# Kernel optimization log

Hardware: AMD Instinct MI355X
Metric: run time of the kernel (lower is better)

The kernel has to match this reference:

```python
import jax, jax.numpy as jnp
import numpy as np

D_MODEL = 1024
D_FF = 4096
LN_EPS = 1e-5


def setup_inputs() -> dict:
    key = jax.random.key(0)
    k_x, k_w1, k_w2 = jax.random.split(key, 3)
    x = jax.random.normal(k_x, (4, 2048, D_MODEL), dtype=jnp.float32)
    # LayerNorm affine params (torch defaults: weight=1, bias=0)
    ln_w = jnp.ones((D_MODEL,), dtype=jnp.float32)
    ln_b = jnp.zeros((D_MODEL,), dtype=jnp.float32)
    # Linear layers, torch default init: U(-1/sqrt(fan_in), 1/sqrt(fan_in))
    lim1 = 1.0 / np.sqrt(D_MODEL)
    w1 = jax.random.uniform(k_w1, (D_MODEL, D_FF), minval=-lim1, maxval=lim1, dtype=jnp.float32)
    b1 = jnp.zeros((D_FF,), dtype=jnp.float32)
    lim2 = 1.0 / np.sqrt(D_FF)
    w2 = jax.random.uniform(k_w2, (D_FF, D_MODEL), minval=-lim2, maxval=lim2, dtype=jnp.float32)
    b2 = jnp.zeros((D_MODEL,), dtype=jnp.float32)
    return {"x": x, "ln_w": ln_w, "ln_b": ln_b, "w1": w1, "b1": b1, "w2": w2, "b2": b2}


def reference(x, ln_w, ln_b, w1, b1, w2, b2):
    # LayerNorm over last dim
    mu = jnp.mean(x, axis=-1, keepdims=True)
    var = jnp.mean(jnp.square(x - mu), axis=-1, keepdims=True)
    h = (x - mu) * jax.lax.rsqrt(var + LN_EPS) * ln_w + ln_b
    # Linear -> ReLU -> Linear
    h = jnp.maximum(jnp.einsum('bsd,df->bsf', h, w1) + b1, 0.0)
    return jnp.einsum('bsf,fd->bsd', h, w2) + b2
```

## Files before the change

### kernel.cpp

```cpp
#include <hip/hip_runtime.h>
#include <stdint.h>

#define D_MODEL 1024
#define D_FF    4096
#define NROWS   8192

typedef __attribute__((ext_vector_type(4))) float f32x4;
typedef __attribute__((ext_vector_type(8))) short short8;

__device__ __forceinline__ unsigned short f2bf(float f) {
  unsigned u = __float_as_uint(f);
  u += 0x7fffu + ((u >> 16) & 1u);
  return (unsigned short)(u >> 16);
}

__global__ __launch_bounds__(256) void ln_bf16_kernel(
    const float* __restrict__ x, const float* __restrict__ lnw,
    const float* __restrict__ lnb, unsigned short* __restrict__ y) {
  const int row = blockIdx.x;
  const int t = threadIdx.x;
  const int w = t >> 6, l = t & 63;
  const float4* xr = (const float4*)(x + (size_t)row * D_MODEL);
  float4 v = xr[t];
  float s  = v.x + v.y + v.z + v.w;
  float s2 = v.x * v.x + v.y * v.y + v.z * v.z + v.w * v.w;
#pragma unroll
  for (int o = 32; o >= 1; o >>= 1) {
    s  += __shfl_xor(s, o);
    s2 += __shfl_xor(s2, o);
  }
  __shared__ float red[8];
  if (l == 0) { red[w] = s; red[4 + w] = s2; }
  __syncthreads();
  s  = red[0] + red[1] + red[2] + red[3];
  s2 = red[4] + red[5] + red[6] + red[7];
  const float mu  = s * (1.0f / D_MODEL);
  const float var = s2 * (1.0f / D_MODEL) - mu * mu;
  const float rs  = rsqrtf(var + 1e-5f);
  float4 wv = ((const float4*)lnw)[t];
  float4 bv = ((const float4*)lnb)[t];
  ushort4 o4;
  o4.x = f2bf((v.x - mu) * rs * wv.x + bv.x);
  o4.y = f2bf((v.y - mu) * rs * wv.y + bv.y);
  o4.z = f2bf((v.z - mu) * rs * wv.z + bv.z);
  o4.w = f2bf((v.w - mu) * rs * wv.w + bv.w);
  *(ushort4*)(y + (size_t)row * D_MODEL + t * 4) = o4;
}

__global__ __launch_bounds__(256) void transpose_f32_bf16(
    const float* __restrict__ src, unsigned short* __restrict__ dst,
    int R, int C) {
  __shared__ float tile[32][33];
  const int tx = threadIdx.x;
  const int ty = threadIdx.y;
  const int r0 = blockIdx.y * 32, c0 = blockIdx.x * 32;
#pragma unroll
  for (int i = 0; i < 32; i += 8)
    tile[ty + i][tx] = src[(size_t)(r0 + ty + i) * C + (c0 + tx)];
  __syncthreads();
#pragma unroll
  for (int i = 0; i < 32; i += 8)
    dst[(size_t)(c0 + ty + i) * R + (r0 + tx)] = f2bf(tile[tx][ty + i]);
}

template <int RELU, int BF16OUT>
__global__ __launch_bounds__(256, 3) void gemm_bt(
    const unsigned short* __restrict__ A, const unsigned short* __restrict__ Bt,
    const float* __restrict__ bias, unsigned short* __restrict__ Cb,
    float* __restrict__ Cf, int M, int N, int K) {
  constexpr int BM = 128, BN = 128, BK = 64;
  __shared__ short lA[BM * BK];
  __shared__ short lB[BN * BK];
  const int t = threadIdx.x;
  const int w = t >> 6, l = t & 63;
  const int bm0 = blockIdx.y * BM, bn0 = blockIdx.x * BN;
  const int wm = (w >> 1) * 64, wn = (w & 1) * 64;

  f32x4 acc[4][4];
  const f32x4 zero = {0.f, 0.f, 0.f, 0.f};
#pragma unroll
  for (int i = 0; i < 4; ++i)
#pragma unroll
    for (int j = 0; j < 4; ++j) acc[i][j] = zero;

  const int nkt = K / BK;
  for (int kt = 0; kt < nkt; ++kt) {
    const int k0 = kt * BK;
#pragma unroll
    for (int p = 0; p < 4; ++p) {
      const int eb = (((p * 4 + w) * 64) + l) * 8;
      const int r = eb >> 6, c = eb & 63;
      __builtin_amdgcn_global_load_lds(
          (const __attribute__((address_space(1))) void*)(A + (size_t)(bm0 + r) * K + (k0 + c)),
          (__attribute__((address_space(3))) void*)(&lA[eb]), 16, 0, 0);
      __builtin_amdgcn_global_load_lds(
          (const __attribute__((address_space(1))) void*)(Bt + (size_t)(bn0 + r) * K + (k0 + c)),
          (__attribute__((address_space(3))) void*)(&lB[eb]), 16, 0, 0);
    }
    __syncthreads();

    const short8* pA = (const short8*)lA;
    const short8* pB = (const short8*)lB;
#pragma unroll
    for (int kb = 0; kb < 2; ++kb) {
      short8 af[4], bfr[4];
      const int kc = kb * 4 + (l >> 4);
#pragma unroll
      for (int f = 0; f < 4; ++f) {
        af[f]  = pA[(wm + f * 16 + (l & 15)) * 8 + kc];
        bfr[f] = pB[(wn + f * 16 + (l & 15)) * 8 + kc];
      }
#pragma unroll
      for (int fm = 0; fm < 4; ++fm)
#pragma unroll
        for (int fn = 0; fn < 4; ++fn)
          acc[fm][fn] = __builtin_amdgcn_mfma_f32_16x16x32_bf16(
              af[fm], bfr[fn], acc[fm][fn], 0, 0, 0);
    }
    __syncthreads();
  }

#pragma unroll
  for (int fn = 0; fn < 4; ++fn) {
    const int n = bn0 + wn + fn * 16 + (l & 15);
    const float bv = bias[n];
#pragma unroll
    for (int fm = 0; fm < 4; ++fm) {
      const int mbase = bm0 + wm + fm * 16 + ((l >> 4) * 4);
#pragma unroll
      for (int j = 0; j < 4; ++j) {
        float v = acc[fm][fn][j] + bv;
        if (RELU) v = v > 0.f ? v : 0.f;
        if (BF16OUT) Cb[(size_t)(mbase + j) * N + n] = f2bf(v);
        else         Cf[(size_t)(mbase + j) * N + n] = v;
      }
    }
  }
}

extern "C" void kernel_launch(void* const* d_in, const int* in_sizes, int n_in,
                              void* d_out, int out_size, void* d_ws, size_t ws_size,
                              hipStream_t stream) {
  const float* x   = (const float*)d_in[0];
  const float* lnw = (const float*)d_in[1];
  const float* lnb = (const float*)d_in[2];
  const float* w1  = (const float*)d_in[3];
  const float* b1  = (const float*)d_in[4];
  const float* w2  = (const float*)d_in[5];
  const float* b2  = (const float*)d_in[6];
  float* out = (float*)d_out;

  char* ws = (char*)d_ws;
  unsigned short* x_ln = (unsigned short*)(ws);
  unsigned short* w1t  = (unsigned short*)(ws + (16u << 20));
  unsigned short* w2t  = (unsigned short*)(ws + (24u << 20));
  unsigned short* h    = (unsigned short*)(ws + (32u << 20));

  ln_bf16_kernel<<<NROWS, 256, 0, stream>>>(x, lnw, lnb, x_ln);
  transpose_f32_bf16<<<dim3(D_FF / 32, D_MODEL / 32), dim3(32, 8), 0, stream>>>(
      w1, w1t, D_MODEL, D_FF);
  transpose_f32_bf16<<<dim3(D_MODEL / 32, D_FF / 32), dim3(32, 8), 0, stream>>>(
      w2, w2t, D_FF, D_MODEL);
  gemm_bt<1, 1><<<dim3(D_FF / 128, NROWS / 128), 256, 0, stream>>>(
      x_ln, w1t, b1, h, nullptr, NROWS, D_FF, D_MODEL);
  gemm_bt<0, 0><<<dim3(D_MODEL / 128, NROWS / 128), 256, 0, stream>>>(
      h, w2t, b2, nullptr, out, NROWS, D_MODEL, D_FF);
}
```

Before: 284.8 us.

## Double-buffer LDS in second GEMM and remap workgroups across XCDs

Adds a PREFETCH template option that double-buffers the A/B LDS tiles, so the next K-tile's global_load_lds is issued before the current tile's MFMAs run, with one barrier per iteration. It is enabled only for the second GEMM (K=4096), and that variant's occupancy hint drops from 3 to 2 blocks because it needs twice the LDS. Both GEMMs also get a workgroup-ID remap that gives each group of 8 consecutive hardware IDs (interleaved across XCDs) a contiguous tile range, for better L2 locality. Risks are lower occupancy and a waitcnt that may stall on the just-issued prefetch before the MFMAs drain.

```diff
diff --git a/kernel.cpp b/kernel.cpp
--- a/kernel.cpp
+++ b/kernel.cpp
@@ -63,17 +63,25 @@
     dst[(size_t)(c0 + ty + i) * R + (r0 + tx)] = f2bf(tile[tx][ty + i]);
 }
 
-template <int RELU, int BF16OUT>
-__global__ __launch_bounds__(256, 3) void gemm_bt(
+template <int RELU, int BF16OUT, int PREFETCH>
+__global__ __launch_bounds__(256, PREFETCH ? 2 : 3) void gemm_bt(
     const unsigned short* __restrict__ A, const unsigned short* __restrict__ Bt,
     const float* __restrict__ bias, unsigned short* __restrict__ Cb,
     float* __restrict__ Cf, int M, int N, int K) {
   constexpr int BM = 128, BN = 128, BK = 64;
-  __shared__ short lA[BM * BK];
-  __shared__ short lB[BN * BK];
+  constexpr int NBUF = PREFETCH ? 2 : 1;
+  __shared__ short lA[NBUF * BM * BK];
+  __shared__ short lB[NBUF * BN * BK];
   const int t = threadIdx.x;
   const int w = t >> 6, l = t & 63;
-  const int bm0 = blockIdx.y * BM, bn0 = blockIdx.x * BN;
+
+  const int gx = gridDim.x;
+  const int nwg = gx * gridDim.y;
+  int id = blockIdx.y * gx + blockIdx.x;
+  id = (id & 7) * (nwg >> 3) + (id >> 3);
+  const int bn0 = (id % gx) * BN;
+  const int bm0 = (id / gx) * BM;
+
   const int wm = (w >> 1) * 64, wn = (w & 1) * 64;
 
   f32x4 acc[4][4];
@@ -83,24 +91,25 @@
 #pragma unroll
     for (int j = 0; j < 4; ++j) acc[i][j] = zero;
 
-  const int nkt = K / BK;
-  for (int kt = 0; kt < nkt; ++kt) {
+  auto stage = [&](int buf, int kt) {
     const int k0 = kt * BK;
+    const int bo = buf * BM * BK;
 #pragma unroll
     for (int p = 0; p < 4; ++p) {
       const int eb = (((p * 4 + w) * 64) + l) * 8;
       const int r = eb >> 6, c = eb & 63;
       __builtin_amdgcn_global_load_lds(
           (const __attribute__((address_space(1))) void*)(A + (size_t)(bm0 + r) * K + (k0 + c)),
-          (__attribute__((address_space(3))) void*)(&lA[eb]), 16, 0, 0);
+          (__attribute__((address_space(3))) void*)(&lA[bo + eb]), 16, 0, 0);
       __builtin_amdgcn_global_load_lds(
           (const __attribute__((address_space(1))) void*)(Bt + (size_t)(bn0 + r) * K + (k0 + c)),
-          (__attribute__((address_space(3))) void*)(&lB[eb]), 16, 0, 0);
+          (__attribute__((address_space(3))) void*)(&lB[bo + eb]), 16, 0, 0);
     }
-    __syncthreads();
+  };
 
-    const short8* pA = (const short8*)lA;
-    const short8* pB = (const short8*)lB;
+  auto compute = [&](int buf) {
+    const short8* pA = (const short8*)&lA[buf * BM * BK];
+    const short8* pB = (const short8*)&lB[buf * BN * BK];
 #pragma unroll
     for (int kb = 0; kb < 2; ++kb) {
       short8 af[4], bfr[4];
@@ -117,7 +126,29 @@
           acc[fm][fn] = __builtin_amdgcn_mfma_f32_16x16x32_bf16(
               af[fm], bfr[fn], acc[fm][fn], 0, 0, 0);
     }
-    __syncthreads();
+  };
+
+  const int nkt = K / BK;
+  if (PREFETCH) {
+    stage(0, 0);
+    asm volatile("s_waitcnt vmcnt(0)" ::: "memory");
+    __builtin_amdgcn_s_barrier();
+    int cur = 0;
+    for (int kt = 0; kt < nkt - 1; ++kt) {
+      stage(cur ^ 1, kt + 1);
+      compute(cur);
+      asm volatile("s_waitcnt vmcnt(0)" ::: "memory");
+      __builtin_amdgcn_s_barrier();
+      cur ^= 1;
+    }
+    compute(cur);
+  } else {
+    for (int kt = 0; kt < nkt; ++kt) {
+      stage(0, kt);
+      __syncthreads();
+      compute(0);
+      __syncthreads();
+    }
   }
 
 #pragma unroll
@@ -161,8 +192,8 @@
       w1, w1t, D_MODEL, D_FF);
   transpose_f32_bf16<<<dim3(D_MODEL / 32, D_FF / 32), dim3(32, 8), 0, stream>>>(
       w2, w2t, D_FF, D_MODEL);
-  gemm_bt<1, 1><<<dim3(D_FF / 128, NROWS / 128), 256, 0, stream>>>(
+  gemm_bt<1, 1, 0><<<dim3(D_FF / 128, NROWS / 128), 256, 0, stream>>>(
       x_ln, w1t, b1, h, nullptr, NROWS, D_FF, D_MODEL);
-  gemm_bt<0, 0><<<dim3(D_MODEL / 128, NROWS / 128), 256, 0, stream>>>(
+  gemm_bt<0, 0, 1><<<dim3(D_MODEL / 128, NROWS / 128), 256, 0, stream>>>(
       h, w2t, b2, nullptr, out, NROWS, D_MODEL, D_FF);
 }
```

Result: slower. 304.3 us (+6.9%).

## Replace GEMM with 8-wave double-buffered pipelined kernel using swizzled LDS

Applied to the files above, without the earlier changes.

Replaces the simple single-buffered 128x128 GEMM with a 512-thread kernel that uses 256-row tiles and double-buffered LDS. Loads are split into half-tile stages that are interleaved with MFMA phases and gated by explicit vmcnt waits. It also adds an XOR swizzle on LDS columns to avoid bank conflicts, a block-id remap meant to improve L2 locality, and raised wave priority around MFMA bursts. The aim is to hide global load latency and raise MFMA utilization, at the cost of more registers and LDS, lower occupancy, and fragile hand-tuned wait counts.

```diff
diff --git a/kernel.cpp b/kernel.cpp
--- a/kernel.cpp
+++ b/kernel.cpp
@@ -12,6 +12,11 @@
   unsigned u = __float_as_uint(f);
   u += 0x7fffu + ((u >> 16) & 1u);
   return (unsigned short)(u >> 16);
+}
+
+template <int N>
+__device__ __forceinline__ void wait_vmcnt() {
+  asm volatile("s_waitcnt vmcnt(%0)" ::"n"(N) : "memory");
 }
 
 __global__ __launch_bounds__(256) void ln_bf16_kernel(
@@ -63,76 +68,146 @@
     dst[(size_t)(c0 + ty + i) * R + (r0 + tx)] = f2bf(tile[tx][ty + i]);
 }
 
-template <int RELU, int BF16OUT>
-__global__ __launch_bounds__(256, 3) void gemm_bt(
+template <int BN, int RELU, int BF16OUT>
+__global__ __launch_bounds__(512, 2) void gemm8p(
     const unsigned short* __restrict__ A, const unsigned short* __restrict__ Bt,
     const float* __restrict__ bias, unsigned short* __restrict__ Cb,
     float* __restrict__ Cf, int M, int N, int K) {
-  constexpr int BM = 128, BN = 128, BK = 64;
-  __shared__ short lA[BM * BK];
-  __shared__ short lB[BN * BK];
+  constexpr int BM = 256;
+  constexpr int FN = BN / 64;
+  constexpr int FNH = FN / 2;
+  constexpr int LA = 2;
+  constexpr int LB = BN / 128;
+  constexpr int AH = 128 * 64;
+  constexpr int BH = (BN / 2) * 64;
+  constexpr int BUFSZ = 2 * AH + 2 * BH;
+  constexpr int RPW = BN / 8;
+  constexpr int WTN = BN / 4;
+  constexpr int NW_A = 2 * LA + LB;
+  constexpr int NW_B = LA + 2 * LB;
+
+  __shared__ short lds[2 * BUFSZ];
+
   const int t = threadIdx.x;
   const int w = t >> 6, l = t & 63;
-  const int bm0 = blockIdx.y * BM, bn0 = blockIdx.x * BN;
-  const int wm = (w >> 1) * 64, wn = (w & 1) * 64;
-
-  f32x4 acc[4][4];
-  const f32x4 zero = {0.f, 0.f, 0.f, 0.f};
-#pragma unroll
-  for (int i = 0; i < 4; ++i)
-#pragma unroll
-    for (int j = 0; j < 4; ++j) acc[i][j] = zero;
-
-  const int nkt = K / BK;
-  for (int kt = 0; kt < nkt; ++kt) {
-    const int k0 = kt * BK;
-#pragma unroll
-    for (int p = 0; p < 4; ++p) {
-      const int eb = (((p * 4 + w) * 64) + l) * 8;
-      const int r = eb >> 6, c = eb & 63;
+  const int wm = w >> 2, wn = w & 3;
+  const int lr = l & 15, lg = l >> 4, l7 = l & 7;
+  const int wm64 = wm * 64, wnr = wn * RPW;
+
+  const int gx = gridDim.x;
+  const int nwg = gx * gridDim.y;
+  int id = blockIdx.y * gx + blockIdx.x;
+  id = (id & 7) * (nwg >> 3) + (id >> 3);
+  const int bn0 = (id % gx) * BN;
+  const int bm0 = (id / gx) * BM;
+
+  f32x4 acc[8][FN];
+#pragma unroll
+  for (int i = 0; i < 8; ++i)
+#pragma unroll
+    for (int j = 0; j < FN; ++j) acc[i][j] = (f32x4){0.f, 0.f, 0.f, 0.f};
+
+  auto stageA = [&](int buf, int mq, int kt) {
+#pragma unroll
+    for (int i = 0; i < LA; ++i) {
+      const int idx = i * 512 + t;
+      const int r = idx >> 3;
+      const int sl = (idx & 7) ^ (r & 7);
+      const int grow = bm0 + ((r >> 6) << 7) + (mq << 6) + (r & 63);
       __builtin_amdgcn_global_load_lds(
-          (const __attribute__((address_space(1))) void*)(A + (size_t)(bm0 + r) * K + (k0 + c)),
-          (__attribute__((address_space(3))) void*)(&lA[eb]), 16, 0, 0);
+          (const __attribute__((address_space(1))) void*)(A + (size_t)grow * K + kt * 64 + sl * 8),
+          (__attribute__((address_space(3))) void*)(&lds[buf * BUFSZ + mq * AH + idx * 8]),
+          16, 0, 0);
+    }
+  };
+  auto stageB = [&](int buf, int nq, int kt) {
+#pragma unroll
+    for (int i = 0; i < LB; ++i) {
+      const int idx = i * 512 + t;
+      const int r = idx >> 3;
+      const int sl = (idx & 7) ^ (r & 7);
+      const int grow = bn0 + (r / RPW) * WTN + nq * RPW + (r % RPW);
       __builtin_amdgcn_global_load_lds(
-          (const __attribute__((address_space(1))) void*)(Bt + (size_t)(bn0 + r) * K + (k0 + c)),
-          (__attribute__((address_space(3))) void*)(&lB[eb]), 16, 0, 0);
+          (const __attribute__((address_space(1))) void*)(Bt + (size_t)grow * K + kt * 64 + sl * 8),
+          (__attribute__((address_space(3))) void*)(&lds[buf * BUFSZ + 2 * AH + nq * BH + idx * 8]),
+          16, 0, 0);
     }
-    __syncthreads();
-
-    const short8* pA = (const short8*)lA;
-    const short8* pB = (const short8*)lB;
-#pragma unroll
-    for (int kb = 0; kb < 2; ++kb) {
-      short8 af[4], bfr[4];
-      const int kc = kb * 4 + (l >> 4);
-#pragma unroll
-      for (int f = 0; f < 4; ++f) {
-        af[f]  = pA[(wm + f * 16 + (l & 15)) * 8 + kc];
-        bfr[f] = pB[(wn + f * 16 + (l & 15)) * 8 + kc];
-      }
-#pragma unroll
-      for (int fm = 0; fm < 4; ++fm)
-#pragma unroll
-        for (int fn = 0; fn < 4; ++fn)
-          acc[fm][fn] = __builtin_amdgcn_mfma_f32_16x16x32_bf16(
-              af[fm], bfr[fn], acc[fm][fn], 0, 0, 0);
-    }
-    __syncthreads();
-  }
-
-#pragma unroll
-  for (int fn = 0; fn < 4; ++fn) {
-    const int n = bn0 + wn + fn * 16 + (l & 15);
-    const float bv = bias[n];
-#pragma unroll
-    for (int fm = 0; fm < 4; ++fm) {
-      const int mbase = bm0 + wm + fm * 16 + ((l >> 4) * 4);
+  };
+
+#define PHASE(MQ, NQ, BUFR, NWAIT, STAGESTMT)                                  \
+  {                                                                            \
+    wait_vmcnt<NWAIT>();                                                       \
+    short8 af[2][4];                                                           \
+    short8 bv[2][FNH];                                                         \
+    _Pragma("unroll") for (int ks = 0; ks < 2; ++ks) {                         \
+      const int sw = (ks << 2) | lg;                                           \
+      _Pragma("unroll") for (int f = 0; f < 4; ++f)                            \
+        af[ks][f] = *(const short8*)&lds[(BUFR) * BUFSZ + (MQ) * AH +          \
+                                         (wm64 + f * 16 + lr) * 64 +           \
+                                         ((sw ^ l7) << 3)];                    \
+      _Pragma("unroll") for (int f = 0; f < FNH; ++f)                          \
+        bv[ks][f] = *(const short8*)&lds[(BUFR) * BUFSZ + 2 * AH + (NQ) * BH + \
+                                         (wnr + f * 16 + lr) * 64 +            \
+                                         ((sw ^ l7) << 3)];                    \
+    }                                                                          \
+    STAGESTMT;                                                                 \
+    __builtin_amdgcn_s_barrier();                                              \
+    asm volatile("s_waitcnt lgkmcnt(0)" ::: "memory");                         \
+    __builtin_amdgcn_sched_barrier(0);                                         \
+    __builtin_amdgcn_s_setprio(1);                                             \
+    _Pragma("unroll") for (int ks = 0; ks < 2; ++ks)                           \
+      _Pragma("unroll") for (int f = 0; f < 4; ++f)                            \
+        _Pragma("unroll") for (int g = 0; g < FNH; ++g)                        \
+          acc[(MQ) * 4 + f][(NQ) * FNH + g] =                                  \
+              __builtin_amdgcn_mfma_f32_16x16x32_bf16(                         \
+                  af[ks][f], bv[ks][g], acc[(MQ) * 4 + f][(NQ) * FNH + g],     \
+                  0, 0, 0);                                                    \
+    __builtin_amdgcn_s_setprio(0);                                             \
+    __builtin_amdgcn_sched_barrier(0);                                         \
+    __builtin_amdgcn_s_barrier();                                              \
+  }
+
+  const int KT_MAX = (K >> 6) - 1;
+  const int NIT = K >> 7;
+
+  stageA(0, 0, 0);
+  stageB(0, 0, 0);
+  stageB(0, 1, 0);
+  stageA(0, 1, 0);
+  stageA(1, 0, 1);
+  stageB(1, 0, 1);
+  wait_vmcnt<2 * LA + 2 * LB>();
+  __builtin_amdgcn_s_barrier();
+
+  for (int it = 0; it < NIT; ++it) {
+    const int k1 = 2 * it + 1;
+    int k2 = 2 * it + 2; k2 = k2 > KT_MAX ? KT_MAX : k2;
+    int k3 = 2 * it + 3; k3 = k3 > KT_MAX ? KT_MAX : k3;
+    PHASE(0, 0, 0, NW_A, stageB(1, 1, k1));
+    PHASE(0, 1, 0, NW_B, stageA(1, 1, k1));
+    PHASE(1, 0, 0, NW_B, stageA(0, 0, k2));
+    PHASE(1, 1, 0, NW_A, stageB(0, 0, k2));
+    PHASE(0, 0, 1, NW_A, stageB(0, 1, k2));
+    PHASE(0, 1, 1, NW_B, stageA(0, 1, k2));
+    PHASE(1, 0, 1, NW_B, stageA(1, 0, k3));
+    PHASE(1, 1, 1, NW_A, stageB(1, 0, k3));
+  }
+#undef PHASE
+  asm volatile("s_waitcnt vmcnt(0)" ::: "memory");
+
+#pragma unroll
+  for (int fn = 0; fn < FN; ++fn) {
+    const int col = bn0 + wn * WTN + fn * 16 + lr;
+    const float bvs = bias[col];
+#pragma unroll
+    for (int fm = 0; fm < 8; ++fm) {
+      const int rb = bm0 + wm * 128 + fm * 16 + lg * 4;
 #pragma unroll
       for (int j = 0; j < 4; ++j) {
-        float v = acc[fm][fn][j] + bv;
+        float v = acc[fm][fn][j] + bvs;
         if (RELU) v = v > 0.f ? v : 0.f;
-        if (BF16OUT) Cb[(size_t)(mbase + j) * N + n] = f2bf(v);
-        else         Cf[(size_t)(mbase + j) * N + n] = v;
+        if (BF16OUT) Cb[(size_t)(rb + j) * N + col] = f2bf(v);
+        else         Cf[(size_t)(rb + j) * N + col] = v;
       }
     }
   }
@@ -161,8 +236,8 @@
       w1, w1t, D_MODEL, D_FF);
   transpose_f32_bf16<<<dim3(D_MODEL / 32, D_FF / 32), dim3(32, 8), 0, stream>>>(
       w2, w2t, D_FF, D_MODEL);
-  gemm_bt<1, 1><<<dim3(D_FF / 128, NROWS / 128), 256, 0, stream>>>(
+  gemm8p<256, 1, 1><<<dim3(D_FF / 256, NROWS / 256), 512, 0, stream>>>(
       x_ln, w1t, b1, h, nullptr, NROWS, D_FF, D_MODEL);
-  gemm_bt<0, 0><<<dim3(D_MODEL / 128, NROWS / 128), 256, 0, stream>>>(
+  gemm8p<128, 0, 0><<<dim3(D_MODEL / 128, NROWS / 256), 512, 0, stream>>>(
       h, w2t, b2, nullptr, out, NROWS, D_MODEL, D_FF);
 }
```

Result: faster. 277.5 us (-2.6%).
